# Optimization experiments

Hardware: AMD Instinct MI355X
Metric: run time of the kernel (lower is better)

The kernel has to match this reference:

```python
import jax, jax.numpy as jnp
import numpy as np

B, S, D, V = 2, 2048, 1024, 50257
GAMMA = 1.0
IGNORE = -100


def setup_inputs() -> dict:
    key = jax.random.key(0)
    k1, k2, k3, k4 = jax.random.split(key, 4)
    embeddings = jax.random.normal(k1, (B, S, D), dtype=jnp.float32)
    W = jax.random.normal(k2, (V, D), dtype=jnp.float32) * (D ** -0.5)
    b = jnp.zeros((V,), dtype=jnp.float32)
    labels = jax.random.randint(k3, (B, S), 0, V, dtype=jnp.int64)
    input_ids = jax.random.randint(k4, (B, S), 0, V, dtype=jnp.int64)
    return {"embeddings": embeddings, "W": W, "b": b, "labels": labels, "input_ids": input_ids}


def _focal_loss(embeddings, W, b, labels):
    # logits: [B, S, V]
    logits = jnp.einsum('bsd,vd->bsv', embeddings, W) + b
    shift_logits = logits[:, :-1, :].reshape(-1, V)          # [N, V]
    shift_labels = labels[:, 1:].reshape(-1)                  # [N]
    valid = shift_labels != IGNORE
    safe = jnp.where(valid, shift_labels, 0)
    logp = jax.nn.log_softmax(shift_logits, axis=-1)
    ce = -jnp.take_along_axis(logp, safe[:, None], axis=-1)[:, 0]
    ce = jnp.where(valid, ce, 0.0)                            # ignore_index -> 0 loss
    pt = jax.lax.stop_gradient(jnp.exp(-ce))
    w = (1.0 - pt) ** GAMMA
    alpha = 1.0 / jnp.mean(w)
    loss = alpha * w * ce
    return jnp.mean(loss)


def reference(embeddings, W, b, labels, input_ids):
    return _focal_loss(embeddings, W, b, labels)
```

## Files before the change

kernel.cpp:

```cpp
#include <hip/hip_runtime.h>
#include <hip/hip_bf16.h>
#include <cstdint>

#define SDIM   2048
#define DDIM   1024
#define VDIM   50257
#define VPAD   50432
#define NROWS  4094
#define MPAD   4096
#define NTM    16
#define NTN    197
#define NCHUNK (NTN * 4)
#define NKT    16
#define IGNORE_IDX (-100)
#define NEGBIG (-3.0e38f)

typedef __bf16 bf16x8 __attribute__((ext_vector_type(8)));
typedef float  f32x4  __attribute__((ext_vector_type(4)));

__device__ static inline unsigned short f2bf(float f) {
    union { float f; uint32_t u; } v; v.f = f;
    uint32_t u = v.u;
    return (unsigned short)((u + 0x7FFFu + ((u >> 16) & 1u)) >> 16);
}

__device__ static inline void gload_lds16(const void* g, void* l) {
    __builtin_amdgcn_global_load_lds(
        (const __attribute__((address_space(1))) unsigned int*)(g),
        (__attribute__((address_space(3))) unsigned int*)(l),
        16, 0, 0);
}

__global__ __launch_bounds__(256) void k_convert_W(const float* __restrict__ W,
                                                   unsigned short* __restrict__ Wb,
                                                   float* __restrict__ acc) {
    if (blockIdx.x == 0 && threadIdx.x < 2) acc[threadIdx.x] = 0.f;
    const int row = blockIdx.x;
    const int c4  = threadIdx.x << 2;
    ushort4 o;
    if (row < VDIM) {
        const float4 f = *(const float4*)(W + (size_t)row * DDIM + c4);
        o.x = f2bf(f.x); o.y = f2bf(f.y); o.z = f2bf(f.z); o.w = f2bf(f.w);
    } else {
        o.x = o.y = o.z = o.w = 0;
    }
    *(ushort4*)(Wb + (size_t)row * DDIM + c4) = o;
}

__global__ __launch_bounds__(256) void k_convert_A(const float* __restrict__ emb,
                                                   unsigned short* __restrict__ Ab) {
    const int row = blockIdx.x;
    const int c4  = threadIdx.x << 2;
    ushort4 o; o.x = o.y = o.z = o.w = 0;
    if (row < NROWS) {
        const int bb = row / 2047;
        const int s  = row - bb * 2047;
        const float4 f = *(const float4*)(emb + ((size_t)bb * SDIM + s) * DDIM + c4);
        o.x = f2bf(f.x); o.y = f2bf(f.y); o.z = f2bf(f.z); o.w = f2bf(f.w);
    }
    *(ushort4*)(Ab + (size_t)row * DDIM + c4) = o;
}

__global__ __launch_bounds__(512, 2) void k_gemm(const unsigned short* __restrict__ Ab,
                                                 const unsigned short* __restrict__ Wb,
                                                 const float* __restrict__ bias,
                                                 float2* __restrict__ Pml) {
    extern __shared__ unsigned short lds[];
    unsigned short* As = lds;
    unsigned short* Bs = lds + 2 * 256 * 64;

    const int tid  = threadIdx.x;
    const int wave = tid >> 6, lane = tid & 63;
    const int q    = lane & 15, g = lane >> 4;
    const int wr   = wave >> 2;
    const int wc   = wave & 3;

    const int bid0 = (int)blockIdx.x;
    const int bid  = (bid0 & 7) * (NTM * NTN / 8) + (bid0 >> 3);
    const int tm   = bid & 15;
    const int tn   = bid >> 4;
    const size_t arow0 = (size_t)tm * 256;
    const size_t brow0 = (size_t)tn * 256;

    f32x4 acc[8][4];
    const f32x4 zf = {0.f, 0.f, 0.f, 0.f};
#pragma unroll
    for (int i = 0; i < 8; ++i)
#pragma unroll
        for (int j = 0; j < 4; ++j) acc[i][j] = zf;

    auto stage_unit = [&](const unsigned short* G, size_t grow0, int kt, int h,
                          unsigned short* L) {
#pragma unroll
        for (int j = 0; j < 2; ++j) {
            const int ci   = j * 512 + tid;
            const int row  = h * 128 + (ci >> 3);
            const int slot = ci & 7;
            const int ss   = slot ^ (row & 7);
            gload_lds16(G + (grow0 + row) * DDIM + kt * 64 + ss * 8,
                        L + h * (128 * 64) + (size_t)(j * 512 + wave * 64) * 8);
        }
    };

    auto phase = [&](int c, int mh, int ks, bool stA, bool stB, int ktn, bool do_vm) {
        const unsigned short* Ac = As + c * (256 * 64);
        const unsigned short* Bc = Bs + c * (256 * 64);
        bf16x8 af[4], bfr[4];
#pragma unroll
        for (int fi = 0; fi < 4; ++fi) {
            const int row = wr * 128 + mh * 64 + fi * 16 + q;
            const int sl  = (ks * 4 + g) ^ (row & 7);
            af[fi] = *(const bf16x8*)(Ac + row * 64 + sl * 8);
        }
#pragma unroll
        for (int fj = 0; fj < 4; ++fj) {
            const int row = wc * 64 + fj * 16 + q;
            const int sl  = (ks * 4 + g) ^ (row & 7);
            bfr[fj] = *(const bf16x8*)(Bc + row * 64 + sl * 8);
        }
        if (stA) {
            stage_unit(Ab, arow0, ktn, 0, As + (c ^ 1) * (256 * 64));
            stage_unit(Ab, arow0, ktn, 1, As + (c ^ 1) * (256 * 64));
        }
        if (stB) {
            stage_unit(Wb, brow0, ktn, 0, Bs + (c ^ 1) * (256 * 64));
            stage_unit(Wb, brow0, ktn, 1, Bs + (c ^ 1) * (256 * 64));
        }
        if (do_vm) asm volatile("s_waitcnt vmcnt(0)" ::: "memory");
        __builtin_amdgcn_sched_barrier(0);
        __builtin_amdgcn_s_barrier();
        asm volatile("s_waitcnt lgkmcnt(0)" ::: "memory");
        __builtin_amdgcn_sched_barrier(0);
        __builtin_amdgcn_s_setprio(1);
#pragma unroll
        for (int fi = 0; fi < 4; ++fi)
#pragma unroll
            for (int fj = 0; fj < 4; ++fj)
                acc[mh * 4 + fi][fj] = __builtin_amdgcn_mfma_f32_16x16x32_bf16(
                    af[fi], bfr[fj], acc[mh * 4 + fi][fj], 0, 0, 0);
        __builtin_amdgcn_s_setprio(0);
        __builtin_amdgcn_sched_barrier(0);
    };

    stage_unit(Ab, arow0, 0, 0, As);
    stage_unit(Ab, arow0, 0, 1, As);
    stage_unit(Wb, brow0, 0, 0, Bs);
    stage_unit(Wb, brow0, 0, 1, Bs);
    asm volatile("s_waitcnt vmcnt(0)" ::: "memory");
    __builtin_amdgcn_sched_barrier(0);
    __builtin_amdgcn_s_barrier();

#pragma unroll 1
    for (int t = 0; t < NKT; ++t) {
        const int  c  = t & 1;
        const bool st = (t < NKT - 1);
        phase(c, 0, 0, st, false, t + 1, false);
        phase(c, 0, 1, false, st, t + 1, false);
        phase(c, 1, 0, false, false, t + 1, false);
        phase(c, 1, 1, false, false, t + 1, true);
    }

    float bv[4]; int colv[4];
#pragma unroll
    for (int fj = 0; fj < 4; ++fj) {
        const int col = tn * 256 + wc * 64 + fj * 16 + q;
        colv[fj] = col;
        bv[fj] = (col < VDIM) ? bias[col] : 0.f;
    }
#pragma unroll
    for (int mf = 0; mf < 8; ++mf) {
#pragma unroll
        for (int r = 0; r < 4; ++r) {
            float vv[4];
#pragma unroll
            for (int fj = 0; fj < 4; ++fj) {
                const float lv = acc[mf][fj][r] + bv[fj];
                vv[fj] = (colv[fj] < VDIM) ? lv : NEGBIG;
            }
            float m = fmaxf(fmaxf(vv[0], vv[1]), fmaxf(vv[2], vv[3]));
#pragma unroll
            for (int mask = 1; mask < 16; mask <<= 1) m = fmaxf(m, __shfl_xor(m, mask));
            float s = __expf(vv[0] - m) + __expf(vv[1] - m) +
                      __expf(vv[2] - m) + __expf(vv[3] - m);
#pragma unroll
            for (int mask = 1; mask < 16; mask <<= 1) s += __shfl_xor(s, mask);
            if (q == ((mf * 4 + r) & 15)) {
                const int rowg = tm * 256 + wr * 128 + mf * 16 + g * 4 + r;
                Pml[(size_t)rowg * NCHUNK + (tn * 4 + wc)] = make_float2(m, s);
            }
        }
    }
}

__global__ __launch_bounds__(256) void k_finalize(const float2* __restrict__ Pml,
                                                  const float* __restrict__ emb,
                                                  const float* __restrict__ W,
                                                  const float* __restrict__ bias,
                                                  const int* __restrict__ labels,
                                                  float* __restrict__ acc) {
    const int r    = blockIdx.x;
    const int tid  = threadIdx.x;
    const int lane = tid & 63, wave = tid >> 6;

    float m = NEGBIG, l = 0.f;
    for (int c = tid; c < NCHUNK; c += 256) {
        const float2 p = Pml[(size_t)r * NCHUNK + c];
        const float mn = fmaxf(m, p.x);
        l = l * __expf(m - mn) + p.y * __expf(p.x - mn);
        m = mn;
    }
#pragma unroll
    for (int mask = 1; mask < 64; mask <<= 1) {
        const float om = __shfl_xor(m, mask);
        const float ol = __shfl_xor(l, mask);
        const float mn = fmaxf(m, om);
        l = l * __expf(m - mn) + ol * __expf(om - mn);
        m = mn;
    }

    const int bb = r / 2047;
    const int s  = r - bb * 2047;
    const int label = labels[bb * SDIM + s + 1];
    const bool valid = (label != IGNORE_IDX);
    const int lab = valid ? label : 0;
    const float* erow = emb + ((size_t)bb * SDIM + s) * DDIM;
    const float* wrow = W + (size_t)lab * DDIM;
    const float4 e  = *(const float4*)(erow + tid * 4);
    const float4 w4 = *(const float4*)(wrow + tid * 4);
    float d = e.x * w4.x + e.y * w4.y + e.z * w4.z + e.w * w4.w;
#pragma unroll
    for (int mask = 1; mask < 64; mask <<= 1) d += __shfl_xor(d, mask);

    __shared__ float sm[4], sl[4], sd[4];
    if (lane == 0) { sm[wave] = m; sl[wave] = l; sd[wave] = d; }
    __syncthreads();
    if (tid == 0) {
        float M = sm[0], L = sl[0];
#pragma unroll
        for (int wv = 1; wv < 4; ++wv) {
            const float mn = fmaxf(M, sm[wv]);
            L = L * __expf(M - mn) + sl[wv] * __expf(sm[wv] - mn);
            M = mn;
        }
        const float dot = sd[0] + sd[1] + sd[2] + sd[3];
        const float lse = M + logf(L);
        const float logit = dot + bias[lab];
        const float ce = valid ? (lse - logit) : 0.f;
        const float pt = __expf(-ce);
        const float w  = valid ? (1.f - pt) : 0.f;
        atomicAdd(acc + 0, w * ce);
        atomicAdd(acc + 1, w);
    }
}

__global__ void k_final(const float* __restrict__ acc, float* __restrict__ out) {
    out[0] = acc[0] / acc[1];
}

extern "C" void kernel_launch(void* const* d_in, const int* in_sizes, int n_in,
                              void* d_out, int out_size, void* d_ws, size_t ws_size,
                              hipStream_t stream) {
    const float* emb    = (const float*)d_in[0];
    const float* W      = (const float*)d_in[1];
    const float* bias   = (const float*)d_in[2];
    const int*   labels = (const int*)d_in[3];

    char* ws = (char*)d_ws;
    const size_t WB = (size_t)VPAD * DDIM * 2;
    const size_t AB = (size_t)MPAD * DDIM * 2;
    const size_t PB = (size_t)MPAD * NCHUNK * 8;
    unsigned short* Wb  = (unsigned short*)ws;
    unsigned short* Ab  = (unsigned short*)(ws + WB);
    float2*         Pml = (float2*)(ws + WB + AB);
    float*          acc = (float*)(ws + WB + AB + PB);

    k_convert_W<<<VPAD, 256, 0, stream>>>(W, Wb, acc);
    k_convert_A<<<MPAD, 256, 0, stream>>>(emb, Ab);
    k_gemm<<<NTM * NTN, 512, 131072, stream>>>(Ab, Wb, bias, Pml);
    k_finalize<<<NROWS, 256, 0, stream>>>(Pml, emb, W, bias, labels, acc);
    k_final<<<1, 1, 0, stream>>>(acc, (float*)d_out);
}
```

Before: 909.8 us.

## Split K-tile staging into half-K slices with partial vmcnt waits in GEMM

The GEMM now stores each 64-wide K tile as two 32-wide slices in LDS, using a new interleaved row layout and swizzle. Each half is staged separately, and waits use s_waitcnt vmcnt(8/4) instead of draining everything at the end of a tile, so global-to-LDS loads overlap more with MFMA work. The W and A conversion kernels also become grid-stride loops with fixed grid sizes, which cuts the number of launched blocks. This adds more complex swizzle indexing and barrier logic, with a risk of subtle races or bank conflicts.

```diff
diff --git a/kernel.cpp b/kernel.cpp
--- a/kernel.cpp
+++ b/kernel.cpp
@@ -14,6 +14,7 @@
 #define NKT    16
 #define IGNORE_IDX (-100)
 #define NEGBIG (-3.0e38f)
+#define SLICE_SH 8192
 
 typedef __bf16 bf16x8 __attribute__((ext_vector_type(8)));
 typedef float  f32x4  __attribute__((ext_vector_type(4)));
@@ -35,30 +36,36 @@
                                                    unsigned short* __restrict__ Wb,
                                                    float* __restrict__ acc) {
     if (blockIdx.x == 0 && threadIdx.x < 2) acc[threadIdx.x] = 0.f;
-    const int row = blockIdx.x;
-    const int c4  = threadIdx.x << 2;
-    ushort4 o;
-    if (row < VDIM) {
-        const float4 f = *(const float4*)(W + (size_t)row * DDIM + c4);
-        o.x = f2bf(f.x); o.y = f2bf(f.y); o.z = f2bf(f.z); o.w = f2bf(f.w);
-    } else {
-        o.x = o.y = o.z = o.w = 0;
-    }
-    *(ushort4*)(Wb + (size_t)row * DDIM + c4) = o;
+    const int nf4 = VPAD * (DDIM / 4);
+    for (int i = blockIdx.x * 256 + threadIdx.x; i < nf4; i += gridDim.x * 256) {
+        const int row = i >> 8;
+        const int c4  = (i & 255) << 2;
+        ushort4 o;
+        if (row < VDIM) {
+            const float4 f = *(const float4*)(W + (size_t)row * DDIM + c4);
+            o.x = f2bf(f.x); o.y = f2bf(f.y); o.z = f2bf(f.z); o.w = f2bf(f.w);
+        } else {
+            o.x = o.y = o.z = o.w = 0;
+        }
+        *(ushort4*)(Wb + (size_t)row * DDIM + c4) = o;
+    }
 }
 
 __global__ __launch_bounds__(256) void k_convert_A(const float* __restrict__ emb,
                                                    unsigned short* __restrict__ Ab) {
-    const int row = blockIdx.x;
-    const int c4  = threadIdx.x << 2;
-    ushort4 o; o.x = o.y = o.z = o.w = 0;
-    if (row < NROWS) {
-        const int bb = row / 2047;
-        const int s  = row - bb * 2047;
-        const float4 f = *(const float4*)(emb + ((size_t)bb * SDIM + s) * DDIM + c4);
-        o.x = f2bf(f.x); o.y = f2bf(f.y); o.z = f2bf(f.z); o.w = f2bf(f.w);
-    }
-    *(ushort4*)(Ab + (size_t)row * DDIM + c4) = o;
+    const int nf4 = MPAD * (DDIM / 4);
+    for (int i = blockIdx.x * 256 + threadIdx.x; i < nf4; i += gridDim.x * 256) {
+        const int row = i >> 8;
+        const int c4  = (i & 255) << 2;
+        ushort4 o; o.x = o.y = o.z = o.w = 0;
+        if (row < NROWS) {
+            const int bb = row / 2047;
+            const int s  = row - bb * 2047;
+            const float4 f = *(const float4*)(emb + ((size_t)bb * SDIM + s) * DDIM + c4);
+            o.x = f2bf(f.x); o.y = f2bf(f.y); o.z = f2bf(f.z); o.w = f2bf(f.w);
+        }
+        *(ushort4*)(Ab + (size_t)row * DDIM + c4) = o;
+    }
 }
 
 __global__ __launch_bounds__(512, 2) void k_gemm(const unsigned short* __restrict__ Ab,
@@ -67,7 +74,7 @@
                                                  float2* __restrict__ Pml) {
     extern __shared__ unsigned short lds[];
     unsigned short* As = lds;
-    unsigned short* Bs = lds + 2 * 256 * 64;
+    unsigned short* Bs = lds + 4 * SLICE_SH;
 
     const int tid  = threadIdx.x;
     const int wave = tid >> 6, lane = tid & 63;
@@ -89,48 +96,49 @@
 #pragma unroll
         for (int j = 0; j < 4; ++j) acc[i][j] = zf;
 
-    auto stage_unit = [&](const unsigned short* G, size_t grow0, int kt, int h,
-                          unsigned short* L) {
+    auto stage_slice = [&](int bufIdx, int kt, int s) {
+        unsigned short* LA = As + (bufIdx * 2 + s) * SLICE_SH;
+        unsigned short* LB = Bs + (bufIdx * 2 + s) * SLICE_SH;
 #pragma unroll
         for (int j = 0; j < 2; ++j) {
-            const int ci   = j * 512 + tid;
-            const int row  = h * 128 + (ci >> 3);
-            const int slot = ci & 7;
-            const int ss   = slot ^ (row & 7);
-            gload_lds16(G + (grow0 + row) * DDIM + kt * 64 + ss * 8,
-                        L + h * (128 * 64) + (size_t)(j * 512 + wave * 64) * 8);
+            const int ci  = j * 512 + tid;
+            const int row = ((ci >> 3) << 1) + ((ci >> 2) & 1);
+            const int cs  = (ci & 3) ^ ((ci >> 3) & 3);
+            const size_t goff = (size_t)kt * 64 + s * 32 + cs * 8;
+            unsigned short* ldst = (unsigned short*)((size_t)(j * 512 + wave * 64) * 8);
+            gload_lds16(Ab + (arow0 + row) * DDIM + goff, LA + (size_t)(j * 512 + wave * 64) * 8);
+            gload_lds16(Wb + (brow0 + row) * DDIM + goff, LB + (size_t)(j * 512 + wave * 64) * 8);
+            (void)ldst;
         }
     };
 
-    auto phase = [&](int c, int mh, int ks, bool stA, bool stB, int ktn, bool do_vm) {
-        const unsigned short* Ac = As + c * (256 * 64);
-        const unsigned short* Bc = Bs + c * (256 * 64);
+    auto lds_frag = [&](const unsigned short* SL, int row) -> bf16x8 {
+        const int line = row >> 1;
+        const int p    = ((row & 1) << 2) + (g ^ (line & 3));
+        return *(const bf16x8*)(SL + line * 64 + p * 8);
+    };
+
+    auto do_phase = [&](int c, int mh, int ks, int stageT, int vm, bool tileEndBar) {
+        if (stageT >= 0) stage_slice(c ^ 1, stageT, ks);
+        if (vm == 8)      { asm volatile("s_waitcnt vmcnt(8)" ::: "memory"); }
+        else if (vm == 4) { asm volatile("s_waitcnt vmcnt(4)" ::: "memory"); }
+        else if (vm == 0) { asm volatile("s_waitcnt vmcnt(0)" ::: "memory"); }
+        if (vm >= 0) {
+            __builtin_amdgcn_sched_barrier(0);
+            __builtin_amdgcn_s_barrier();
+        }
+        const unsigned short* SA = As + (c * 2 + ks) * SLICE_SH;
+        const unsigned short* SB = Bs + (c * 2 + ks) * SLICE_SH;
         bf16x8 af[4], bfr[4];
 #pragma unroll
-        for (int fi = 0; fi < 4; ++fi) {
-            const int row = wr * 128 + mh * 64 + fi * 16 + q;
-            const int sl  = (ks * 4 + g) ^ (row & 7);
-            af[fi] = *(const bf16x8*)(Ac + row * 64 + sl * 8);
-        }
-#pragma unroll
-        for (int fj = 0; fj < 4; ++fj) {
-            const int row = wc * 64 + fj * 16 + q;
-            const int sl  = (ks * 4 + g) ^ (row & 7);
-            bfr[fj] = *(const bf16x8*)(Bc + row * 64 + sl * 8);
-        }
-        if (stA) {
-            stage_unit(Ab, arow0, ktn, 0, As + (c ^ 1) * (256 * 64));
-            stage_unit(Ab, arow0, ktn, 1, As + (c ^ 1) * (256 * 64));
-        }
-        if (stB) {
-            stage_unit(Wb, brow0, ktn, 0, Bs + (c ^ 1) * (256 * 64));
-            stage_unit(Wb, brow0, ktn, 1, Bs + (c ^ 1) * (256 * 64));
-        }
-        if (do_vm) asm volatile("s_waitcnt vmcnt(0)" ::: "memory");
-        __builtin_amdgcn_sched_barrier(0);
-        __builtin_amdgcn_s_barrier();
+        for (int fi = 0; fi < 4; ++fi)
+            af[fi] = lds_frag(SA, wr * 128 + mh * 64 + fi * 16 + q);
+#pragma unroll
+        for (int fj = 0; fj < 4; ++fj)
+            bfr[fj] = lds_frag(SB, wc * 64 + fj * 16 + q);
         asm volatile("s_waitcnt lgkmcnt(0)" ::: "memory");
         __builtin_amdgcn_sched_barrier(0);
+        if (tileEndBar) __builtin_amdgcn_s_barrier();
         __builtin_amdgcn_s_setprio(1);
 #pragma unroll
         for (int fi = 0; fi < 4; ++fi)
@@ -142,22 +150,23 @@
         __builtin_amdgcn_sched_barrier(0);
     };
 
-    stage_unit(Ab, arow0, 0, 0, As);
-    stage_unit(Ab, arow0, 0, 1, As);
-    stage_unit(Wb, brow0, 0, 0, Bs);
-    stage_unit(Wb, brow0, 0, 1, Bs);
-    asm volatile("s_waitcnt vmcnt(0)" ::: "memory");
-    __builtin_amdgcn_sched_barrier(0);
-    __builtin_amdgcn_s_barrier();
+    stage_slice(0, 0, 0);
+    stage_slice(0, 0, 1);
 
 #pragma unroll 1
-    for (int t = 0; t < NKT; ++t) {
-        const int  c  = t & 1;
-        const bool st = (t < NKT - 1);
-        phase(c, 0, 0, st, false, t + 1, false);
-        phase(c, 0, 1, false, st, t + 1, false);
-        phase(c, 1, 0, false, false, t + 1, false);
-        phase(c, 1, 1, false, false, t + 1, true);
+    for (int t = 0; t < NKT - 1; ++t) {
+        const int c = t & 1;
+        do_phase(c, 0, 0, t + 1, 8, false);
+        do_phase(c, 1, 0, -1, -1, false);
+        do_phase(c, 0, 1, t + 1, 8, false);
+        do_phase(c, 1, 1, -1, -1, true);
+    }
+    {
+        const int c = (NKT - 1) & 1;
+        do_phase(c, 0, 0, -1, 4, false);
+        do_phase(c, 1, 0, -1, -1, false);
+        do_phase(c, 0, 1, -1, 0, false);
+        do_phase(c, 1, 1, -1, -1, false);
     }
 
     float bv[4]; int colv[4];
@@ -274,8 +283,8 @@
     float2*         Pml = (float2*)(ws + WB + AB);
     float*          acc = (float*)(ws + WB + AB + PB);
 
-    k_convert_W<<<VPAD, 256, 0, stream>>>(W, Wb, acc);
-    k_convert_A<<<MPAD, 256, 0, stream>>>(emb, Ab);
+    k_convert_W<<<2048, 256, 0, stream>>>(W, Wb, acc);
+    k_convert_A<<<1024, 256, 0, stream>>>(emb, Ab);
     k_gemm<<<NTM * NTN, 512, 131072, stream>>>(Ab, Wb, bias, Pml);
     k_finalize<<<NROWS, 256, 0, stream>>>(Pml, emb, W, bias, labels, acc);
     k_final<<<1, 1, 0, stream>>>(acc, (float*)d_out);
```

New measurement: 944.1 us. 3.8% more time.
